# Performance work log

Measured on AMD Instinct MI355X. Metric: run time of the kernel, lower is better.

Reference implementation:

```python
import jax, jax.numpy as jnp
import numpy as np

N = 4096      # batch size (PK-sampled)
D = 1024      # feature dim
K = 4         # instances per identity
NUM_IDS = N // K


def setup_inputs() -> dict:
    key = jax.random.key(0)
    inputs = jax.random.normal(key, (N, D), dtype=jnp.float32)
    # PK-structured labels: NUM_IDS identities, K instances each.
    targets = jnp.repeat(jnp.arange(NUM_IDS, dtype=jnp.int32), K)
    # Flags alternate within each identity -> every (same/diff id) x (same/diff flag)
    # combination is non-empty for every anchor row.
    flags = jnp.tile(jnp.array([0, 1, 0, 1], dtype=jnp.int32), N // 4)
    epoch = 10  # unused by the loss, kept for signature fidelity
    return {"inputs": inputs, "targets": targets, "flags": flags, "epoch": epoch}


def reference(inputs, targets, flags, epoch):
    # Pairwise Euclidean distances: ||a||^2 + ||b||^2 - 2 a.b, clamped + sqrt.
    sq = jnp.sum(inputs * inputs, axis=1, keepdims=True)          # [n,1]
    dist = sq + sq.T - 2.0 * (inputs @ inputs.T)                   # [n,n]
    dist = jnp.sqrt(jnp.clip(dist, 1e-12, None))

    same_id = targets[:, None] == targets[None, :]                 # mask_1
    same_fl = flags[:, None] == flags[None, :]                     # mask_2
    m_same_hp = same_id & same_fl
    m_same_hn = (~same_id) & same_fl
    m_dif_hp = same_id & (~same_fl)
    m_dif_hn = (~same_id) & (~same_fl)

    NEG = jnp.asarray(-jnp.inf, dist.dtype)
    POS = jnp.asarray(jnp.inf, dist.dtype)
    dist_same_ap = jnp.max(jnp.where(m_same_hp, dist, NEG), axis=1)
    dist_same_an = jnp.min(jnp.where(m_same_hn, dist, POS), axis=1)
    dist_dif_ap = jnp.max(jnp.where(m_dif_hp, dist, NEG), axis=1)
    dist_dif_an = jnp.min(jnp.where(m_dif_hn, dist, POS), axis=1)

    # torch: first index in the FULL row equal to the masked min (exact equality)
    same_min_idx = jnp.argmax(dist == dist_same_an[:, None], axis=1)  # [n]
    dif_min_idx = jnp.argmax(dist == dist_dif_an[:, None], axis=1)    # [n]
    dist_dif_neg = dist[same_min_idx, dif_min_idx]                    # [n]

    relu = jax.nn.relu
    # MarginRankingLoss(x1, x2, y=1) = mean(relu(x2 - x1 + margin))
    loss_same = jnp.mean(relu(dist_same_ap - dist_same_an + 0.8))
    loss_dif = jnp.mean(relu(dist_dif_ap - dist_dif_an + 0.5))
    loss_neg = jnp.mean(relu(dist_same_ap - dist_dif_neg + 0.3))
    return loss_same + loss_dif + loss_neg
```

## Files before the change

### kernel.cpp

```cpp
#include <hip/hip_runtime.h>

#define NROWS 4096
#define DIM   1024

using f32x4 = __attribute__((ext_vector_type(4))) float;
using bfrag = __attribute__((ext_vector_type(8))) short;

__device__ __forceinline__ unsigned short f2bf(float f) {
  unsigned u = __float_as_uint(f);
  u += 0x7fffu + ((u >> 16) & 1u);
  return (unsigned short)(u >> 16);
}
__device__ __forceinline__ float bf2f(unsigned short b) {
  return __uint_as_float(((unsigned)b) << 16);
}
__device__ __forceinline__ unsigned long long shflx64(unsigned long long v, int m) {
  int lo = __shfl_xor((int)(unsigned)(v & 0xffffffffull), m);
  int hi = __shfl_xor((int)(unsigned)(v >> 32), m);
  return ((unsigned long long)(unsigned)hi << 32) | (unsigned)lo;
}

__global__ void prep_kernel(const float* __restrict__ X, unsigned short* __restrict__ Xb,
                            float* __restrict__ sqv, int* maxS, int* maxD,
                            unsigned long long* minS, unsigned long long* minD,
                            float* out) {
  int row = blockIdx.x, t = threadIdx.x;
  float4 v = reinterpret_cast<const float4*>(X + (size_t)row * DIM)[t];
  unsigned short b0 = f2bf(v.x), b1 = f2bf(v.y), b2 = f2bf(v.z), b3 = f2bf(v.w);
  float f0 = bf2f(b0), f1 = bf2f(b1), f2 = bf2f(b2), f3 = bf2f(b3);
  float s = f0 * f0 + f1 * f1 + f2 * f2 + f3 * f3;
  reinterpret_cast<ushort4*>(Xb + (size_t)row * DIM)[t] = make_ushort4(b0, b1, b2, b3);
  for (int m = 32; m; m >>= 1) s += __shfl_xor(s, m);
  __shared__ float ws4[4];
  if ((t & 63) == 0) ws4[t >> 6] = s;
  __syncthreads();
  if (t == 0) {
    sqv[row] = (ws4[0] + ws4[1]) + (ws4[2] + ws4[3]);
    maxS[row] = 0; maxD[row] = 0; minS[row] = ~0ull; minD[row] = ~0ull;
    if (row == 0) out[0] = 0.f;
  }
}

#define STAGE(KS)                                                                \
  {                                                                              \
    _Pragma("unroll")                                                            \
    for (int qq = 0; qq < 4; ++qq) {                                             \
      int boff = (wave * 4 + qq) * 1024;                     \
      int r = (wave * 4 + qq) * 8 + (lane >> 3);        \
      const unsigned short* sA = Xb + (size_t)(row0 + r) * DIM + (KS) + ksrc;    \
      __builtin_amdgcn_global_load_lds(                                          \
          (const __attribute__((address_space(1))) void*)sA,                     \
          (__attribute__((address_space(3))) void*)(smem + boff), 16, 0, 0);     \
      const unsigned short* sB = Xb + (size_t)(col0 + r) * DIM + (KS) + ksrc;    \
      __builtin_amdgcn_global_load_lds(                                          \
          (const __attribute__((address_space(1))) void*)sB,                     \
          (__attribute__((address_space(3))) void*)(smem + 16384 + boff), 16, 0, 0); \
    }                                                                            \
  }

__global__ __launch_bounds__(256) void gram_kernel(
    const unsigned short* __restrict__ Xb, const float* __restrict__ sqv,
    const int* __restrict__ tg, const int* __restrict__ fl,
    int* maxS, int* maxD, unsigned long long* minS, unsigned long long* minD) {
  __shared__ __attribute__((aligned(16))) char smem[32768];
  __shared__ float srow[128], scol[128];
  __shared__ int rtagp[128], ctagp[128];

  int tm = 0, g = blockIdx.x, rem = 32;
  while (g >= rem) { g -= rem; rem--; tm++; }
  int tn = tm + g;
  const int row0 = tm * 128, col0 = tn * 128;
  const int tid = threadIdx.x;
  const int wave = tid >> 6, lane = tid & 63;
  const int q = lane >> 4, li = lane & 15;
  const int ksrc = ((lane & 7) ^ (lane >> 3)) * 8;

  if (tid < 128) {
    srow[tid] = sqv[row0 + tid];
    rtagp[tid] = (fl[row0 + tid] << 12) | tg[row0 + tid];
  } else {
    int c = tid - 128;
    scol[c] = sqv[col0 + c];
    ctagp[c] = (fl[col0 + c] << 12) | tg[col0 + c];
  }

  unsigned short (*As)[64] = (unsigned short (*)[64])smem;
  unsigned short (*Bs)[64] = (unsigned short (*)[64])(smem + 16384);

  f32x4 acc[4][4] = {};
  const int wr = (wave >> 1) * 64, wc = (wave & 1) * 64;

  for (int ks = 0; ks < DIM; ks += 64) {
    __syncthreads();
    STAGE(ks);
    __syncthreads();
#pragma unroll
    for (int kk = 0; kk < 2; ++kk) {
      bfrag a[4], b[4];
      int kel = ((kk * 4 + q) ^ (lane & 7)) * 8;
#pragma unroll
      for (int m = 0; m < 4; ++m)
        a[m] = *(const bfrag*)&As[wr + m * 16 + li][kel];
#pragma unroll
      for (int n = 0; n < 4; ++n)
        b[n] = *(const bfrag*)&Bs[wc + n * 16 + li][kel];
#pragma unroll
      for (int m = 0; m < 4; ++m)
#pragma unroll
        for (int n = 0; n < 4; ++n)
          acc[m][n] = __builtin_amdgcn_mfma_f32_16x16x32_bf16(a[m], b[n], acc[m][n], 0, 0, 0);
    }
  }

  float cmxS[4], cmxD[4];
  unsigned long long cmnS[4], cmnD[4];
  int ctv[4]; float scv[4];
#pragma unroll
  for (int n = 0; n < 4; ++n) {
    cmxS[n] = -1.f; cmxD[n] = -1.f; cmnS[n] = ~0ull; cmnD[n] = ~0ull;
    int lc = wc + n * 16 + li; ctv[n] = ctagp[lc]; scv[n] = scol[lc];
  }
#pragma unroll
  for (int m = 0; m < 4; ++m)
#pragma unroll
    for (int r = 0; r < 4; ++r) {
      int lr = wr + m * 16 + q * 4 + r;
      int rt = rtagp[lr];
      float sr = srow[lr];
      unsigned long long rbase = (unsigned)(row0 + lr);
      float rmxS = -1.f, rmxD = -1.f;
      unsigned long long rmnS = ~0ull, rmnD = ~0ull;
#pragma unroll
      for (int n = 0; n < 4; ++n) {
        float d = sqrtf(fmaxf(sr + scv[n] - 2.0f * acc[m][n][r], 1e-12f));
        int x = rt ^ ctv[n];
        unsigned long long db = (unsigned long long)__float_as_uint(d) << 32;
        unsigned long long pkr = db | (unsigned)(col0 + wc + n * 16 + li);
        unsigned long long pkc = db | rbase;
        if ((x & 0xFFF) == 0) {
          if ((x >> 12) == 0) { rmxS = fmaxf(rmxS, d); cmxS[n] = fmaxf(cmxS[n], d); }
          else                { rmxD = fmaxf(rmxD, d); cmxD[n] = fmaxf(cmxD[n], d); }
        } else {
          if ((x >> 12) == 0) { if (pkr < rmnS) rmnS = pkr; if (pkc < cmnS[n]) cmnS[n] = pkc; }
          else                { if (pkr < rmnD) rmnD = pkr; if (pkc < cmnD[n]) cmnD[n] = pkc; }
        }
      }
#pragma unroll
      for (int mk = 1; mk <= 8; mk <<= 1) {
        rmxS = fmaxf(rmxS, __shfl_xor(rmxS, mk));
        rmxD = fmaxf(rmxD, __shfl_xor(rmxD, mk));
        unsigned long long o = shflx64(rmnS, mk); if (o < rmnS) rmnS = o;
        o = shflx64(rmnD, mk); if (o < rmnD) rmnD = o;
      }
      if (li == 0) {
        int gr = row0 + lr;
        atomicMax(&maxS[gr], __float_as_int(rmxS));
        atomicMax(&maxD[gr], __float_as_int(rmxD));
        atomicMin(&minS[gr], rmnS);
        atomicMin(&minD[gr], rmnD);
      }
    }
#pragma unroll
  for (int n = 0; n < 4; ++n) {
#pragma unroll
    for (int mk = 16; mk <= 32; mk <<= 1) {
      cmxS[n] = fmaxf(cmxS[n], __shfl_xor(cmxS[n], mk));
      cmxD[n] = fmaxf(cmxD[n], __shfl_xor(cmxD[n], mk));
      unsigned long long o = shflx64(cmnS[n], mk); if (o < cmnS[n]) cmnS[n] = o;
      o = shflx64(cmnD[n], mk); if (o < cmnD[n]) cmnD[n] = o;
    }
    if (lane < 16) {
      int gc = col0 + wc + n * 16 + lane;
      atomicMax(&maxS[gc], __float_as_int(cmxS[n]));
      atomicMax(&maxD[gc], __float_as_int(cmxD[n]));
      atomicMin(&minS[gc], cmnS[n]);
      atomicMin(&minD[gc], cmnD[n]);
    }
  }
}

__global__ void finish_kernel(const unsigned short* __restrict__ Xb,
                              const float* __restrict__ sqv,
                              const int* __restrict__ maxS, const int* __restrict__ maxD,
                              const unsigned long long* __restrict__ minS,
                              const unsigned long long* __restrict__ minD, float* out) {
  int wave = threadIdx.x >> 6, lane = threadIdx.x & 63;
  float part = 0.f;
  for (int rr = 0; rr < 8; ++rr) {
    int row = blockIdx.x * 32 + wave * 8 + rr;
    unsigned long long pS = minS[row], pD = minD[row];
    int ia = (int)(pS & 0xffffffffull);
    int ib = (int)(pD & 0xffffffffull);
    const ushort4* pa = (const ushort4*)(Xb + (size_t)ia * DIM);
    const ushort4* pb = (const ushort4*)(Xb + (size_t)ib * DIM);
    float s = 0.f;
#pragma unroll
    for (int qq = 0; qq < 4; ++qq) {
      ushort4 a = pa[lane + qq * 64], b = pb[lane + qq * 64];
      s += bf2f(a.x) * bf2f(b.x) + bf2f(a.y) * bf2f(b.y) +
           bf2f(a.z) * bf2f(b.z) + bf2f(a.w) * bf2f(b.w);
    }
    for (int m = 32; m; m >>= 1) s += __shfl_xor(s, m);
    if (lane == 0) {
      float dneg = sqrtf(fmaxf(sqv[ia] + sqv[ib] - 2.f * s, 1e-12f));
      float mS = __int_as_float(maxS[row]);
      float mD = __int_as_float(maxD[row]);
      float mnSv = __uint_as_float((unsigned)(pS >> 32));
      float mnDv = __uint_as_float((unsigned)(pD >> 32));
      part += fmaxf(mS - mnSv + 0.8f, 0.f) + fmaxf(mD - mnDv + 0.5f, 0.f) +
              fmaxf(mS - dneg + 0.3f, 0.f);
    }
  }
  __shared__ float wp[4];
  if (lane == 0) wp[wave] = part;
  __syncthreads();
  if (threadIdx.x == 0)
    atomicAdd(out, ((wp[0] + wp[1]) + (wp[2] + wp[3])) * (1.0f / 4096.0f));
}

extern "C" void kernel_launch(void* const* d_in, const int* in_sizes, int n_in,
                              void* d_out, int out_size, void* d_ws, size_t ws_size,
                              hipStream_t stream) {
  const float* X = (const float*)d_in[0];
  const int* tg  = (const int*)d_in[1];
  const int* fl  = (const int*)d_in[2];
  float* out = (float*)d_out;

  char* w = (char*)d_ws;
  unsigned short* Xb = (unsigned short*)(w);
  float* sqv = (float*)(w + 8388608);
  int* maxS  = (int*)(w + 8404992);
  int* maxD  = (int*)(w + 8421376);
  unsigned long long* minS = (unsigned long long*)(w + 8437760);
  unsigned long long* minD = (unsigned long long*)(w + 8470528);

  prep_kernel<<<NROWS, 256, 0, stream>>>(X, Xb, sqv, maxS, maxD, minS, minD, out);
  gram_kernel<<<528, 256, 0, stream>>>(Xb, sqv, tg, fl, maxS, maxD, minS, minD);
  finish_kernel<<<128, 256, 0, stream>>>(Xb, sqv, maxS, maxD, minS, minD, out);
}
```

Baseline: 149.5 us.

## Replace global atomics with per-tile partial tables and a separate reduction kernel

Each gram tile now merges its per-row and per-column max/min results in shared memory and writes one partial record per row/column to a global table, with no global atomics. A new finstats kernel reduces the partials for each row across all tiles that touch it, and the loss kernel reads the precomputed stats. This removes contended 64-bit atomicMin/atomicMax traffic and the init writes in prep. In exchange it adds an extra kernel launch and a few MB of partial-table traffic, and the reduction kernel runs only 32 blocks.

```diff
diff --git a/kernel.cpp b/kernel.cpp
--- a/kernel.cpp
+++ b/kernel.cpp
@@ -2,9 +2,11 @@
 
 #define NROWS 4096
 #define DIM   1024
+#define NT    528
 
 using f32x4 = __attribute__((ext_vector_type(4))) float;
 using bfrag = __attribute__((ext_vector_type(8))) short;
+typedef unsigned long long u64;
 
 __device__ __forceinline__ unsigned short f2bf(float f) {
   unsigned u = __float_as_uint(f);
@@ -14,16 +16,14 @@
 __device__ __forceinline__ float bf2f(unsigned short b) {
   return __uint_as_float(((unsigned)b) << 16);
 }
-__device__ __forceinline__ unsigned long long shflx64(unsigned long long v, int m) {
+__device__ __forceinline__ u64 shflx64(u64 v, int m) {
   int lo = __shfl_xor((int)(unsigned)(v & 0xffffffffull), m);
   int hi = __shfl_xor((int)(unsigned)(v >> 32), m);
-  return ((unsigned long long)(unsigned)hi << 32) | (unsigned)lo;
+  return ((u64)(unsigned)hi << 32) | (unsigned)lo;
 }
 
 __global__ void prep_kernel(const float* __restrict__ X, unsigned short* __restrict__ Xb,
-                            float* __restrict__ sqv, int* maxS, int* maxD,
-                            unsigned long long* minS, unsigned long long* minD,
-                            float* out) {
+                            float* __restrict__ sqv, float* out) {
   int row = blockIdx.x, t = threadIdx.x;
   float4 v = reinterpret_cast<const float4*>(X + (size_t)row * DIM)[t];
   unsigned short b0 = f2bf(v.x), b1 = f2bf(v.y), b2 = f2bf(v.z), b3 = f2bf(v.w);
@@ -36,7 +36,6 @@
   __syncthreads();
   if (t == 0) {
     sqv[row] = (ws4[0] + ws4[1]) + (ws4[2] + ws4[3]);
-    maxS[row] = 0; maxD[row] = 0; minS[row] = ~0ull; minD[row] = ~0ull;
     if (row == 0) out[0] = 0.f;
   }
 }
@@ -61,7 +60,8 @@
 __global__ __launch_bounds__(256) void gram_kernel(
     const unsigned short* __restrict__ Xb, const float* __restrict__ sqv,
     const int* __restrict__ tg, const int* __restrict__ fl,
-    int* maxS, int* maxD, unsigned long long* minS, unsigned long long* minD) {
+    float* __restrict__ PmS, float* __restrict__ PmD,
+    u64* __restrict__ PnS, u64* __restrict__ PnD) {
   __shared__ __attribute__((aligned(16))) char smem[32768];
   __shared__ float srow[128], scol[128];
   __shared__ int rtagp[128], ctagp[128];
@@ -111,9 +111,15 @@
           acc[m][n] = __builtin_amdgcn_mfma_f32_16x16x32_bf16(a[m], b[n], acc[m][n], 0, 0, 0);
     }
   }
+  __syncthreads();
+
+  float* tab_mS = (float*)smem;
+  float* tab_mD = (float*)(smem + 2048);
+  u64*   tab_nS = (u64*)(smem + 4096);
+  u64*   tab_nD = (u64*)(smem + 8192);
 
   float cmxS[4], cmxD[4];
-  unsigned long long cmnS[4], cmnD[4];
+  u64 cmnS[4], cmnD[4];
   int ctv[4]; float scv[4];
 #pragma unroll
   for (int n = 0; n < 4; ++n) {
@@ -127,16 +133,16 @@
       int lr = wr + m * 16 + q * 4 + r;
       int rt = rtagp[lr];
       float sr = srow[lr];
-      unsigned long long rbase = (unsigned)(row0 + lr);
+      u64 rbase = (unsigned)(row0 + lr);
       float rmxS = -1.f, rmxD = -1.f;
-      unsigned long long rmnS = ~0ull, rmnD = ~0ull;
+      u64 rmnS = ~0ull, rmnD = ~0ull;
 #pragma unroll
       for (int n = 0; n < 4; ++n) {
         float d = sqrtf(fmaxf(sr + scv[n] - 2.0f * acc[m][n][r], 1e-12f));
         int x = rt ^ ctv[n];
-        unsigned long long db = (unsigned long long)__float_as_uint(d) << 32;
-        unsigned long long pkr = db | (unsigned)(col0 + wc + n * 16 + li);
-        unsigned long long pkc = db | rbase;
+        u64 db = (u64)__float_as_uint(d) << 32;
+        u64 pkr = db | (unsigned)(col0 + wc + n * 16 + li);
+        u64 pkc = db | rbase;
         if ((x & 0xFFF) == 0) {
           if ((x >> 12) == 0) { rmxS = fmaxf(rmxS, d); cmxS[n] = fmaxf(cmxS[n], d); }
           else                { rmxD = fmaxf(rmxD, d); cmxD[n] = fmaxf(cmxD[n], d); }
@@ -149,15 +155,13 @@
       for (int mk = 1; mk <= 8; mk <<= 1) {
         rmxS = fmaxf(rmxS, __shfl_xor(rmxS, mk));
         rmxD = fmaxf(rmxD, __shfl_xor(rmxD, mk));
-        unsigned long long o = shflx64(rmnS, mk); if (o < rmnS) rmnS = o;
+        u64 o = shflx64(rmnS, mk); if (o < rmnS) rmnS = o;
         o = shflx64(rmnD, mk); if (o < rmnD) rmnD = o;
       }
       if (li == 0) {
-        int gr = row0 + lr;
-        atomicMax(&maxS[gr], __float_as_int(rmxS));
-        atomicMax(&maxD[gr], __float_as_int(rmxD));
-        atomicMin(&minS[gr], rmnS);
-        atomicMin(&minD[gr], rmnD);
+        int slot = lr * 2 + (wave & 1);
+        tab_mS[slot] = rmxS; tab_mD[slot] = rmxD;
+        tab_nS[slot] = rmnS; tab_nD[slot] = rmnD;
       }
     }
 #pragma unroll
@@ -166,31 +170,70 @@
     for (int mk = 16; mk <= 32; mk <<= 1) {
       cmxS[n] = fmaxf(cmxS[n], __shfl_xor(cmxS[n], mk));
       cmxD[n] = fmaxf(cmxD[n], __shfl_xor(cmxD[n], mk));
-      unsigned long long o = shflx64(cmnS[n], mk); if (o < cmnS[n]) cmnS[n] = o;
+      u64 o = shflx64(cmnS[n], mk); if (o < cmnS[n]) cmnS[n] = o;
       o = shflx64(cmnD[n], mk); if (o < cmnD[n]) cmnD[n] = o;
     }
     if (lane < 16) {
-      int gc = col0 + wc + n * 16 + lane;
-      atomicMax(&maxS[gc], __float_as_int(cmxS[n]));
-      atomicMax(&maxD[gc], __float_as_int(cmxD[n]));
-      atomicMin(&minS[gc], cmnS[n]);
-      atomicMin(&minD[gc], cmnD[n]);
-    }
-  }
-}
-
-__global__ void finish_kernel(const unsigned short* __restrict__ Xb,
-                              const float* __restrict__ sqv,
-                              const int* __restrict__ maxS, const int* __restrict__ maxD,
-                              const unsigned long long* __restrict__ minS,
-                              const unsigned long long* __restrict__ minD, float* out) {
+      int lc = wc + n * 16 + lane;
+      int slot = 256 + lc * 2 + (wave >> 1);
+      tab_mS[slot] = cmxS[n]; tab_mD[slot] = cmxD[n];
+      tab_nS[slot] = cmnS[n]; tab_nD[slot] = cmnD[n];
+    }
+  }
+  __syncthreads();
+  {
+    int e = tid;
+    float mS = fmaxf(tab_mS[2 * e], tab_mS[2 * e + 1]);
+    float mD = fmaxf(tab_mD[2 * e], tab_mD[2 * e + 1]);
+    u64 a = tab_nS[2 * e], b = tab_nS[2 * e + 1]; u64 nS = a < b ? a : b;
+    a = tab_nD[2 * e]; b = tab_nD[2 * e + 1]; u64 nD = a < b ? a : b;
+    size_t o = (size_t)blockIdx.x * 256 + e;
+    PmS[o] = mS; PmD[o] = mD; PnS[o] = nS; PnD[o] = nD;
+  }
+}
+
+__global__ void finstats_kernel(const float* __restrict__ PmS, const float* __restrict__ PmD,
+                                const u64* __restrict__ PnS, const u64* __restrict__ PnD,
+                                float* __restrict__ stP, float* __restrict__ stM,
+                                int* __restrict__ stIA, int* __restrict__ stIB) {
+  int r = blockIdx.x * 128 + threadIdx.x;
+  int p = r >> 7, rl = r & 127;
+  float mS = -1.f, mD = -1.f;
+  u64 nS = ~0ull, nD = ~0ull;
+  int g0 = p * 32 - (p * (p - 1)) / 2;
+  for (int t = 0; t < 32 - p; ++t) {
+    size_t base = (size_t)(g0 + t) * 256 + rl;
+    mS = fmaxf(mS, PmS[base]); mD = fmaxf(mD, PmD[base]);
+    u64 a = PnS[base]; if (a < nS) nS = a;
+    u64 b = PnD[base]; if (b < nD) nD = b;
+  }
+  int gg = p;
+  for (int t = 0; t <= p; ++t) {
+    size_t base = (size_t)gg * 256 + 128 + rl;
+    mS = fmaxf(mS, PmS[base]); mD = fmaxf(mD, PmD[base]);
+    u64 a = PnS[base]; if (a < nS) nS = a;
+    u64 b = PnD[base]; if (b < nD) nD = b;
+    gg += 31 - t;
+  }
+  float mnSv = __uint_as_float((unsigned)(nS >> 32));
+  float mnDv = __uint_as_float((unsigned)(nD >> 32));
+  stP[r] = fmaxf(mS - mnSv + 0.8f, 0.f) + fmaxf(mD - mnDv + 0.5f, 0.f);
+  stM[r] = mS;
+  stIA[r] = (int)(nS & 0xffffffffull);
+  stIB[r] = (int)(nD & 0xffffffffull);
+}
+
+__global__ void finloss_kernel(const unsigned short* __restrict__ Xb,
+                               const float* __restrict__ sqv,
+                               const float* __restrict__ stP, const float* __restrict__ stM,
+                               const int* __restrict__ stIA, const int* __restrict__ stIB,
+                               float* out) {
   int wave = threadIdx.x >> 6, lane = threadIdx.x & 63;
   float part = 0.f;
   for (int rr = 0; rr < 8; ++rr) {
     int row = blockIdx.x * 32 + wave * 8 + rr;
-    unsigned long long pS = minS[row], pD = minD[row];
-    int ia = (int)(pS & 0xffffffffull);
-    int ib = (int)(pD & 0xffffffffull);
+    int ia = stIA[row];
+    int ib = stIB[row];
     const ushort4* pa = (const ushort4*)(Xb + (size_t)ia * DIM);
     const ushort4* pb = (const ushort4*)(Xb + (size_t)ib * DIM);
     float s = 0.f;
@@ -203,12 +246,7 @@
     for (int m = 32; m; m >>= 1) s += __shfl_xor(s, m);
     if (lane == 0) {
       float dneg = sqrtf(fmaxf(sqv[ia] + sqv[ib] - 2.f * s, 1e-12f));
-      float mS = __int_as_float(maxS[row]);
-      float mD = __int_as_float(maxD[row]);
-      float mnSv = __uint_as_float((unsigned)(pS >> 32));
-      float mnDv = __uint_as_float((unsigned)(pD >> 32));
-      part += fmaxf(mS - mnSv + 0.8f, 0.f) + fmaxf(mD - mnDv + 0.5f, 0.f) +
-              fmaxf(mS - dneg + 0.3f, 0.f);
+      part += stP[row] + fmaxf(stM[row] - dneg + 0.3f, 0.f);
     }
   }
   __shared__ float wp[4];
@@ -229,12 +267,17 @@
   char* w = (char*)d_ws;
   unsigned short* Xb = (unsigned short*)(w);
   float* sqv = (float*)(w + 8388608);
-  int* maxS  = (int*)(w + 8404992);
-  int* maxD  = (int*)(w + 8421376);
-  unsigned long long* minS = (unsigned long long*)(w + 8437760);
-  unsigned long long* minD = (unsigned long long*)(w + 8470528);
-
-  prep_kernel<<<NROWS, 256, 0, stream>>>(X, Xb, sqv, maxS, maxD, minS, minD, out);
-  gram_kernel<<<528, 256, 0, stream>>>(Xb, sqv, tg, fl, maxS, maxD, minS, minD);
-  finish_kernel<<<128, 256, 0, stream>>>(Xb, sqv, maxS, maxD, minS, minD, out);
-}
+  float* PmS = (float*)(w + 8404992);
+  float* PmD = (float*)(w + 8945664);
+  u64*   PnS = (u64*)(w + 9486336);
+  u64*   PnD = (u64*)(w + 10567680);
+  float* stP = (float*)(w + 11649024);
+  float* stM = (float*)(w + 11665408);
+  int*   stIA = (int*)(w + 11681792);
+  int*   stIB = (int*)(w + 11698176);
+
+  prep_kernel<<<NROWS, 256, 0, stream>>>(X, Xb, sqv, out);
+  gram_kernel<<<NT, 256, 0, stream>>>(Xb, sqv, tg, fl, PmS, PmD, PnS, PnD);
+  finstats_kernel<<<32, 128, 0, stream>>>(PmS, PmD, PnS, PnD, stP, stM, stIA, stIB);
+  finloss_kernel<<<128, 256, 0, stream>>>(Xb, sqv, stP, stM, stIA, stIB, out);
+}
```

New measurement: 164.3 us, median of 2. 1.1x slower.
